# Optimization experiments

Hardware: AMD Instinct MI355X
Metric: run time of the kernel (lower is better)

Reference implementation:

```python
import jax, jax.numpy as jnp
import numpy as np

KH, KW = 3, 3
STRIDE = (1, 1)
PAD = ((1, 1), (1, 1))
WEIGHT_BIT = 8


def asym_quant_params(num_bits, smin, smax):
    # ZeroQ asymmetric_linear_quantization_params (signed, integral zero point)
    n = 2.0 ** num_bits - 1.0
    scale = n / jnp.maximum(smax - smin, 1e-8)
    zero_point = jnp.round(scale * smin) + 2.0 ** (num_bits - 1)
    return scale, zero_point


def setup_inputs() -> dict:
    key = jax.random.key(0)
    k1, k2, k3 = jax.random.split(key, 3)
    x = jax.random.normal(k1, (16, 128, 56, 56), dtype=jnp.float32)
    weight = jax.random.normal(k2, (128, 128, 3, 3), dtype=jnp.float32) * 0.05
    bias = jax.random.normal(k3, (128,), dtype=jnp.float32) * 0.1
    return {"x": x, "weight": weight, "bias": bias, "activation_bit": 8}


def reference(x, weight, bias, activation_bit):
    B, C, H, W = x.shape
    Cout = weight.shape[0]

    # nn.functional.unfold(x, 3, stride=1, padding=1).transpose(1, 2)
    # conv_general_dilated_patches emits feature dim ordered (c, kh, kw),
    # matching torch unfold's channel-major layout.
    patches = jax.lax.conv_general_dilated_patches(
        x, filter_shape=(KH, KW), window_strides=STRIDE, padding=PAD)
    _, F, OH, OW = patches.shape          # F = C*KH*KW
    L = OH * OW
    calc_x = patches.reshape(B, F, L).transpose(0, 2, 1)  # [B, L, F]

    # ----- weight quantization: per-output-channel asymmetric int8 -----
    w2 = weight.reshape(Cout, -1)                          # [Cout, F]
    w_min = w2.min(axis=1)
    w_max = w2.max(axis=1)
    scale_w, zp_w = asym_quant_params(WEIGHT_BIT, w_min, w_max)  # [Cout]
    nw = 2.0 ** (WEIGHT_BIT - 1)
    qw = jnp.clip(jnp.round(scale_w[:, None] * w2 - zp_w[:, None]), -nw, nw - 1)

    # ----- activation quantization: per-tensor asymmetric -----
    x_min = calc_x.min()
    x_max = calc_x.max()
    scale_x, zp_x = asym_quant_params(activation_bit, x_min, x_max)
    nx = 2.0 ** (activation_bit - 1)
    qx = jnp.clip(jnp.round(scale_x * calc_x - zp_x), -nx, nx - 1)  # [B, L, F]

    # bias: linear_quantize(bias, scale_w*scale_x, 0)
    qb = jnp.round(scale_w * scale_x * bias)                # [Cout]

    # integer matmul + asymmetric zero-point correction
    # real value r ~= (q + zp) / scale, so
    # x.w*sx*sw = qx.qw + zp_w*sum(qx) + zp_x*sum(qw) + K*zp_w*zp_x
    mult_res = jnp.einsum('blf,of->blo', qx, qw)            # [B, L, Cout]
    K = w2.shape[1]
    res = (mult_res
           + zp_w * qx.sum(-1, keepdims=True)               # [B, L, 1]*[Cout]
           + zp_x * qw.sum(axis=1)                          # [Cout]
           + K * zp_w * zp_x
           + qb)                                            # [B, L, Cout]

    # requantize accumulator to activation_bit bits, then dequantize
    r_min, r_max = res.min(), res.max()
    scale_r, zp_r = asym_quant_params(activation_bit, r_min, r_max)
    nr = 2.0 ** (activation_bit - 1)
    qr = jnp.clip(jnp.round(scale_r * res - zp_r), -nr, nr - 1)
    out = (qr + zp_r) / scale_r / (scale_w * scale_x)       # [B, L, Cout]

    return out.transpose(0, 2, 1)                           # [B, Cout, L]
```

## Files before the change

kernel.cpp:

```cpp
#include <hip/hip_runtime.h>
#include <stdint.h>

#pragma clang fp contract(off)

typedef __attribute__((ext_vector_type(4))) int i32x4;
typedef __attribute__((ext_vector_type(16))) int i32x16;

#define B_    16
#define C_    128
#define HW_   56
#define L_    3136
#define CO_   128
#define F_    1152
#define M_    50176
#define NT_   784

#define OFF_PBMIN 0
#define OFF_PBMAX 3136
#define OFF_PRMIN 6272
#define OFF_PRMAX 9408
#define OFF_SW    12544
#define OFF_ZPW   13056
#define OFF_CNT   14080
#define OFF_QS    15616
#define OFF_QW    16384
#define OFF_QX    163840
#define OFF_S     6586368
#define OFF_RES   6787072

__device__ __forceinline__ int read_abit(const int* p) {
    int i = *p;
    if (i > 0 && i < 32) return i;
    float f = __int_as_float(i);
    int fi = (int)f;
    return (fi > 0 && fi < 32) ? fi : 8;
}

__device__ __forceinline__ int swz_tile(int blk) {
    return (blk & 7) * 98 + (blk >> 3);
}

__device__ __forceinline__ void gsync(char* ws, int sp) {
    unsigned* base = (unsigned*)(ws + OFF_CNT) + sp * 128;
    __syncthreads();
    if (threadIdx.x == 0) {
        __threadfence();
        atomicAdd(&base[(blockIdx.x & 7) * 16], 1u);
    }
    if (threadIdx.x < 8) {
        while (__hip_atomic_load(&base[threadIdx.x * 16],
                                 __ATOMIC_RELAXED, __HIP_MEMORY_SCOPE_AGENT) < 98u)
            __builtin_amdgcn_s_sleep(2);
    }
    __threadfence();
    __syncthreads();
}

__device__ __forceinline__ void block_fminmax(float& mn, float& mx, float* sred) {
    for (int m = 32; m; m >>= 1) {
        mn = fminf(mn, __shfl_xor(mn, m));
        mx = fmaxf(mx, __shfl_xor(mx, m));
    }
    int w = threadIdx.x >> 6;
    if ((threadIdx.x & 63) == 0) { sred[w] = mn; sred[4 + w] = mx; }
    __syncthreads();
    mn = fminf(fminf(sred[0], sred[1]), fminf(sred[2], sred[3]));
    mx = fmaxf(fmaxf(sred[4], sred[5]), fmaxf(sred[6], sred[7]));
    __syncthreads();
}
__device__ __forceinline__ void block_iminmax(int& mn, int& mx, int* ired) {
    for (int m = 32; m; m >>= 1) {
        mn = min(mn, __shfl_xor(mn, m));
        mx = max(mx, __shfl_xor(mx, m));
    }
    int w = threadIdx.x >> 6;
    if ((threadIdx.x & 63) == 0) { ired[w] = mn; ired[4 + w] = mx; }
    __syncthreads();
    mn = min(min(ired[0], ired[1]), min(ired[2], ired[3]));
    mx = max(max(ired[4], ired[5]), max(ired[6], ired[7]));
    __syncthreads();
}
__device__ __forceinline__ int block_isum(int v, int* ired) {
    for (int m = 32; m; m >>= 1) v += __shfl_xor(v, m);
    int w = threadIdx.x >> 6;
    if ((threadIdx.x & 63) == 0) ired[w] = v;
    __syncthreads();
    v = ired[0] + ired[1] + ired[2] + ired[3];
    __syncthreads();
    return v;
}

__device__ __forceinline__ void dev_p1(const float4* __restrict__ x4, int n4,
                                       char* ws, float* sred) {
    float mn = 0.0f, mx = 0.0f;
    int stride = gridDim.x * blockDim.x;
    for (int i = blockIdx.x * blockDim.x + threadIdx.x; i < n4; i += stride) {
        float4 v = x4[i];
        mn = fminf(mn, fminf(fminf(v.x, v.y), fminf(v.z, v.w)));
        mx = fmaxf(mx, fmaxf(fmaxf(v.x, v.y), fmaxf(v.z, v.w)));
    }
    block_fminmax(mn, mx, sred);
    if (threadIdx.x == 0) {
        ((float*)(ws + OFF_PBMIN))[blockIdx.x] = mn;
        ((float*)(ws + OFF_PBMAX))[blockIdx.x] = mx;
    }
}

__device__ __forceinline__ void dev_p1w(const float* __restrict__ wgt,
                                        char* ws, float* sred, int* ired) {
    int o = blockIdx.x;
    const float* wr = wgt + o * F_;
    float mn = 3.4e38f, mx = -3.4e38f;
    for (int f = threadIdx.x; f < F_; f += 256) {
        float v = wr[f];
        mn = fminf(mn, v); mx = fmaxf(mx, v);
    }
    block_fminmax(mn, mx, sred);
    float sw = 255.0f / fmaxf(mx - mn, 1e-8f);
    float zw = rintf(sw * mn) + 128.0f;
    signed char* qw = (signed char*)(ws + OFF_QW);
    int qsum = 0;
    for (int f = threadIdx.x; f < F_; f += 256) {
        float q = fminf(fmaxf(rintf(sw * wr[f] - zw), -128.0f), 127.0f);
        int qi = (int)q;
        qsum += qi;
        int c = f / 9, j = f - c * 9;
        qw[j * 16384 + (c >> 4) * 2048 + (o << 4) + (c & 15)] = (signed char)qi;
    }
    qsum = block_isum(qsum, ired);
    if (threadIdx.x == 0) {
        ((int*)(ws + OFF_QS))[o]  = qsum;
        ((int*)(ws + OFF_ZPW))[o] = (int)zw;
        ((float*)(ws + OFF_SW))[o] = sw;
    }
}

__device__ __forceinline__ void dev_reduce_pb(const char* ws, float* sred,
                                              float& xmin, float& xmax) {
    const float* pbmin = (const float*)(ws + OFF_PBMIN);
    const float* pbmax = (const float*)(ws + OFF_PBMAX);
    float mn = 0.0f, mx = 0.0f;
    for (int i = threadIdx.x; i < NT_; i += 256) {
        mn = fminf(mn, pbmin[i]);
        mx = fmaxf(mx, pbmax[i]);
    }
    block_fminmax(mn, mx, sred);
    xmin = mn; xmax = mx;
}

__device__ __forceinline__ void dev_reduce_pr(const char* ws, int* ired,
                                              int& rmin, int& rmax) {
    const int* prmin = (const int*)(ws + OFF_PRMIN);
    const int* prmax = (const int*)(ws + OFF_PRMAX);
    int mn = INT32_MAX, mx = INT32_MIN;
    for (int i = threadIdx.x; i < NT_; i += 256) {
        mn = min(mn, prmin[i]);
        mx = max(mx, prmax[i]);
    }
    block_iminmax(mn, mx, ired);
    rmin = mn; rmax = mx;
}

__device__ __forceinline__ void dev_p2x(const float* __restrict__ x, char* ws, char* pool,
                                        float sx, float zx, int nx) {
    int (*ssum)[64] = (int(*)[64])pool;
    float lo = -(float)nx, hif = (float)(nx - 1);
    signed char* qxt = (signed char*)(ws + OFF_QX);
    int gid = swz_tile(blockIdx.x);
    int b = gid / 49, lcq = gid - b * 49;
    int l0 = lcq * 64;
    int t = threadIdx.x, lane = t & 63, cgp = t >> 6;
    int l = l0 + lane;
    const float* xb = x + ((size_t)b * C_) * L_ + l;
    int4* dst = (int4*)(qxt + ((size_t)(b * L_ + l)) * 128);
    int psum = 0;
    #pragma unroll
    for (int ii = 0; ii < 2; ++ii) {
        int c16 = (cgp + 4 * ii) * 16;
        int wds[4];
        #pragma unroll
        for (int k = 0; k < 4; ++k) {
            int wv = 0;
            #pragma unroll
            for (int e = 0; e < 4; ++e) {
                int c = c16 + 4 * k + e;
                float v = xb[(size_t)c * L_];
                int qi = (int)fminf(fmaxf(rintf(sx * v - zx), lo), hif);
                psum += qi;
                wv |= (qi & 255) << (8 * e);
            }
            wds[k] = wv;
        }
        int4 vv; vv.x = wds[0]; vv.y = wds[1]; vv.z = wds[2]; vv.w = wds[3];
        dst[c16 >> 4] = vv;
    }
    ssum[cgp][lane] = psum;
    __syncthreads();
    if (cgp == 0) {
        int* S = (int*)(ws + OFF_S);
        S[b * L_ + l] = ssum[0][lane] + ssum[1][lane] + ssum[2][lane] + ssum[3][lane];
    }
    __syncthreads();
}

template <bool WRITE_RES>
__device__ __forceinline__ void dev_p3(char* __restrict__ ws, char* pool, int* ired,
                                       const float* __restrict__ bias,
                                       int abit, float sx, float zx,
                                       i32x16& acc0, i32x16& acc1) {
    signed char* As = (signed char*)pool;
    signed char* Bs = (signed char*)(pool + 8192);
    int* S_s = (int*)(pool + 24576);
    int* sq  = (int*)(pool + 25504);
    const signed char* qxt = (const signed char*)(ws + OFF_QX);
    const signed char* qw  = (const signed char*)(ws + OFF_QW);
    const int* Sg  = (const int*)(ws + OFF_S);
    const int* zpw = (const int*)(ws + OFF_ZPW);

    int t = threadIdx.x;
    int mg = swz_tile(blockIdx.x) * 64;
    int b = mg / L_, l0 = mg - b * L_;
    int prow0 = l0 / HW_;
    int nx = 1 << (abit - 1);
    int q0 = min(max(-(int)zx, -nx), nx - 1);
    int pw = (q0 & 255) * 0x01010101;
    int4 pad4; pad4.x = pw; pad4.y = pw; pad4.z = pw; pad4.w = pw;
    int padS = C_ * q0;
    const signed char* qxtb = qxt + (size_t)b * L_ * 128;
    const int* Sb = Sg + b * L_;

    int chA = t & 7, rowA0 = t >> 3, rowA1 = rowA0 + 32;
    int li0 = l0 + rowA0, li1 = l0 + rowA1;
    int oh0 = li0 / HW_, ow0 = li0 - oh0 * HW_;
    int oh1 = li1 / HW_, ow1 = li1 - oh1 * HW_;

    int4 a0, a1, br0, br1, br2, br3;
    #define P3_LOAD_A(J) do {                                                          \
        int kh = (J) / 3 - 1, kw = (J) % 3 - 1;                                        \
        int ih = oh0 + kh, iw = ow0 + kw;                                              \
        a0 = ((unsigned)ih < HW_ && (unsigned)iw < HW_)                                \
             ? *(const int4*)(qxtb + ((ih * HW_ + iw) << 7) + (chA << 4)) : pad4;      \
        ih = oh1 + kh; iw = ow1 + kw;                                                  \
        a1 = ((unsigned)ih < HW_ && (unsigned)iw < HW_)                                \
             ? *(const int4*)(qxtb + ((ih * HW_ + iw) << 7) + (chA << 4)) : pad4;      \
    } while (0)
    #define P3_LOAD_B(J) do {                                                          \
        const int4* src = (const int4*)(qw + (J) * 16384);                             \
        br0 = src[t]; br1 = src[256 + t]; br2 = src[512 + t]; br3 = src[768 + t];      \
    } while (0)

    P3_LOAD_A(0); P3_LOAD_B(0);
    if (t < 232) {
        int ri = t / 58, c1 = t - ri * 58;
        int ih = prow0 - 1 + ri, iw = c1 - 1;
        S_s[t] = ((unsigned)ih < HW_ && (unsigned)iw < HW_) ? Sb[ih * HW_ + iw] : padS;
    }
    __syncthreads();
    if (t < 64) {
        int l = l0 + t;
        int oh = l / HW_, ow = l - oh * HW_;
        int ri = oh - prow0 + 1, ci = ow + 1;
        int s = 0;
        #pragma unroll
        for (int dr = -1; dr <= 1; ++dr)
            #pragma unroll
            for (int dc = -1; dc <= 1; ++dc)
                s += S_s[(ri + dr) * 58 + ci + dc];
        sq[t] = s;
    }

    int lane = t & 63, w = t >> 6;
    int wm = (w >> 1) << 5, wn = (w & 1) << 6;
    int r = lane & 31, hi = lane >> 5;
    #pragma unroll
    for (int i = 0; i < 16; ++i) { acc0[i] = 0; acc1[i] = 0; }

    #pragma unroll
    for (int j = 0; j < 9; ++j) {
        if (j > 0) __syncthreads();
        *(int4*)&As[(rowA0 << 7) + ((chA ^ (rowA0 & 7)) << 4)] = a0;
        *(int4*)&As[(rowA1 << 7) + ((chA ^ (rowA1 & 7)) << 4)] = a1;
        {
            int4* d = (int4*)Bs;
            d[t] = br0; d[256 + t] = br1; d[512 + t] = br2; d[768 + t] = br3;
        }
        if (j < 8) { P3_LOAD_A(j + 1); P3_LOAD_B(j + 1); }
        __syncthreads();
        i32x4 af[4], bf0[4], bf1[4];
        #pragma unroll
        for (int kk = 0; kk < 4; ++kk) {
            int ch2 = kk * 2 + hi, row = wm + r;
            af[kk]  = *(const i32x4*)&As[(row << 7) + ((ch2 ^ (row & 7)) << 4)];
            bf0[kk] = *(const i32x4*)&Bs[ch2 * 2048 + ((wn + r) << 4)];
            bf1[kk] = *(const i32x4*)&Bs[ch2 * 2048 + ((wn + 32 + r) << 4)];
        }
        #pragma unroll
        for (int kk = 0; kk < 4; ++kk) {
            acc0 = __builtin_amdgcn_mfma_i32_32x32x32_i8(af[kk], bf0[kk], acc0, 0, 0, 0);
            acc1 = __builtin_amdgcn_mfma_i32_32x32x32_i8(af[kk], bf1[kk], acc1, 0, 0, 0);
        }
    }
    #undef P3_LOAD_A
    #undef P3_LOAD_B

    int o0 = wn + r, o1 = wn + 32 + r;
    const int* qs = (const int*)(ws + OFF_QS);
    const float* swp = (const float*)(ws + OFF_SW);
    int zxi = (int)zx;
    int zw0 = zpw[o0], zw1 = zpw[o1];
    int c0 = zxi * qs[o0] + F_ * zw0 * zxi + (int)rintf(swp[o0] * sx * bias[o0]);
    int c1 = zxi * qs[o1] + F_ * zw1 * zxi + (int)rintf(swp[o1] * sx * bias[o1]);
    int lmin = INT32_MAX, lmax = INT32_MIN;
    int* resp = (int*)(ws + OFF_RES);
    #pragma unroll
    for (int g = 0; g < 16; ++g) {
        int row = wm + (g & 3) + ((g >> 2) << 3) + (hi << 2);
        int s = sq[row];
        int v0 = acc0[g] + zw0 * s + c0;
        int v1 = acc1[g] + zw1 * s + c1;
        acc0[g] = v0; acc1[g] = v1;
        lmin = min(lmin, min(v0, v1));
        lmax = max(lmax, max(v0, v1));
        if (WRITE_RES) {
            int m = mg + row;
            resp[m * CO_ + o0] = v0;
            resp[m * CO_ + o1] = v1;
        }
    }
    block_iminmax(lmin, lmax, ired);
    if (t == 0) {
        ((int*)(ws + OFF_PRMIN))[blockIdx.x] = lmin;
        ((int*)(ws + OFF_PRMAX))[blockIdx.x] = lmax;
    }
    __syncthreads();
}

__device__ __forceinline__ void dev_p4(const char* ws, char* pool, float* __restrict__ out,
                                       int abit, float sx, int rmin, int rmax,
                                       const i32x16& acc0, const i32x16& acc1) {
    const float* scale_w = (const float*)(ws + OFF_SW);
    float* tile = (float*)pool;
    int t = threadIdx.x;
    int mg = swz_tile(blockIdx.x) * 64;
    int b = mg / L_, l0 = mg - b * L_;
    int lane = t & 63, w = t >> 6;
    int wm = (w >> 1) << 5, wn = (w & 1) << 6;
    int r = lane & 31, hi = lane >> 5;
    int o0 = wn + r, o1 = wn + 32 + r;
    int nx = 1 << (abit - 1);
    float nlev = (float)((1 << abit) - 1);
    float rminf = (float)rmin, rmaxf = (float)rmax;
    float sr = nlev / fmaxf(rmaxf - rminf, 1e-8f);
    float zr = rintf(sr * rminf) + (float)nx;
    float lo = -(float)nx, hiq = (float)(nx - 1);
    float swsx0 = scale_w[o0] * sx, swsx1 = scale_w[o1] * sx;
    #pragma unroll
    for (int g = 0; g < 16; ++g) {
        int row = wm + (g & 3) + ((g >> 2) << 3) + (hi << 2);
        float qa = fminf(fmaxf(rintf(sr * (float)acc0[g] - zr), lo), hiq);
        float qb = fminf(fmaxf(rintf(sr * (float)acc1[g] - zr), lo), hiq);
        tile[row * 129 + o0] = ((qa + zr) / sr) / swsx0;
        tile[row * 129 + o1] = ((qb + zr) / sr) / swsx1;
    }
    __syncthreads();
    #pragma unroll
    for (int i = 0; i < 8; ++i) {
        int o = (t >> 4) + i * 16;
        int l4 = (t & 15) * 4;
        float4 f;
        #pragma unroll
        for (int jj = 0; jj < 4; ++jj)
            ((float*)&f)[jj] = tile[(l4 + jj) * 129 + o];
        *(float4*)(out + ((size_t)(b * CO_ + o)) * L_ + l0 + l4) = f;
    }
}

__global__ __launch_bounds__(256, 4) void k_fused(const float* __restrict__ x,
                                                  const float* __restrict__ wgt,
                                                  const float* __restrict__ bias,
                                                  const int* __restrict__ abit_p,
                                                  char* __restrict__ ws,
                                                  float* __restrict__ out) {
    __shared__ __align__(16) char pool[33280];
    __shared__ float sred[8];
    __shared__ int ired[8];

    int n4 = (B_ * C_ * L_) / 4;
    dev_p1((const float4*)x, n4, ws, sred);
    if (blockIdx.x < CO_) dev_p1w(wgt, ws, sred, ired);
    gsync(ws, 0);

    float xmin, xmax;
    dev_reduce_pb(ws, sred, xmin, xmax);
    int abit = read_abit(abit_p);
    float nlv = (float)((1 << abit) - 1);
    float sx = nlv / fmaxf(xmax - xmin, 1e-8f);
    float zx = rintf(sx * xmin) + (float)(1 << (abit - 1));
    int nx = 1 << (abit - 1);
    dev_p2x(x, ws, pool, sx, zx, nx);
    gsync(ws, 1);

    i32x16 acc0, acc1;
    dev_p3<false>(ws, pool, ired, bias, abit, sx, zx, acc0, acc1);
    gsync(ws, 2);

    int rmin, rmax;
    dev_reduce_pr(ws, ired, rmin, rmax);
    dev_p4(ws, pool, out, abit, sx, rmin, rmax, acc0, acc1);
}

__global__ __launch_bounds__(256) void fb_p1(const float4* __restrict__ x4, int n4,
                                             const float* __restrict__ wgt,
                                             char* __restrict__ ws) {
    __shared__ float sred[8];
    __shared__ int ired[8];
    dev_p1(x4, n4, ws, sred);
    if (blockIdx.x < CO_) dev_p1w(wgt, ws, sred, ired);
}

__global__ __launch_bounds__(256) void fb_p2(const float* __restrict__ x,
                                             const int* __restrict__ abit_p,
                                             char* __restrict__ ws) {
    __shared__ __align__(16) char pool[1024];
    __shared__ float sred[8];
    float xmin, xmax;
    dev_reduce_pb(ws, sred, xmin, xmax);
    int abit = read_abit(abit_p);
    float nlv = (float)((1 << abit) - 1);
    float sx = nlv / fmaxf(xmax - xmin, 1e-8f);
    float zx = rintf(sx * xmin) + (float)(1 << (abit - 1));
    int nx = 1 << (abit - 1);
    dev_p2x(x, ws, pool, sx, zx, nx);
}

__global__ __launch_bounds__(256, 4) void fb_p3(const float* __restrict__ bias,
                                                const int* __restrict__ abit_p,
                                                char* __restrict__ ws) {
    __shared__ __align__(16) char pool[25760];
    __shared__ float sred[8];
    __shared__ int ired[8];
    float xmin, xmax;
    dev_reduce_pb(ws, sred, xmin, xmax);
    int abit = read_abit(abit_p);
    float nlv = (float)((1 << abit) - 1);
    float sx = nlv / fmaxf(xmax - xmin, 1e-8f);
    float zx = rintf(sx * xmin) + (float)(1 << (abit - 1));
    i32x16 acc0, acc1;
    dev_p3<true>(ws, pool, ired, bias, abit, sx, zx, acc0, acc1);
}

__global__ __launch_bounds__(256) void fb_p4(const int* __restrict__ abit_p,
                                             char* __restrict__ ws,
                                             float* __restrict__ out) {
    __shared__ int tile[64 * 65];
    __shared__ float sred[8];
    __shared__ int ired[8];
    float xmin, xmax;
    dev_reduce_pb(ws, sred, xmin, xmax);
    int abit = read_abit(abit_p);
    float nlv = (float)((1 << abit) - 1);
    float sxv = nlv / fmaxf(xmax - xmin, 1e-8f);
    int rmin, rmax;
    dev_reduce_pr(ws, ired, rmin, rmax);

    const int* res = (const int*)(ws + OFF_RES);
    const float* scale_w = (const float*)(ws + OFF_SW);
    int t = threadIdx.x;
    int bid = blockIdx.x;
    int lcq = bid % 49; int tmp2 = bid / 49; int ocq = tmp2 & 1; int b = tmp2 >> 1;
    int l0 = lcq * 64, o0 = ocq * 64;

    const int* resb = res + ((size_t)(b * L_ + l0)) * CO_ + o0;
    #pragma unroll
    for (int i = 0; i < 4; ++i) {
        int lr = (t >> 4) + i * 16;
        int oc4 = (t & 15) * 4;
        int4 v = *(const int4*)(resb + lr * CO_ + oc4);
        int* d = &tile[lr * 65 + oc4];
        d[0] = v.x; d[1] = v.y; d[2] = v.z; d[3] = v.w;
    }
    int nxq = 1 << (abit - 1);
    float rminf = (float)rmin, rmaxf = (float)rmax;
    float sr = nlv / fmaxf(rmaxf - rminf, 1e-8f);
    float zr = rintf(sr * rminf) + (float)nxq;
    float lo = -(float)nxq, hiq = (float)(nxq - 1);
    __syncthreads();
    #pragma unroll
    for (int i = 0; i < 4; ++i) {
        int o = (t >> 4) + i * 16;
        int l4 = (t & 15) * 4;
        float swsx = scale_w[o0 + o] * sxv;
        float4 f;
        #pragma unroll
        for (int jj = 0; jj < 4; ++jj) {
            int rv = tile[(l4 + jj) * 65 + o];
            float q = fminf(fmaxf(rintf(sr * (float)rv - zr), lo), hiq);
            ((float*)&f)[jj] = ((q + zr) / sr) / swsx;
        }
        *(float4*)(out + ((size_t)(b * CO_ + o0 + o)) * L_ + l0 + l4) = f;
    }
}


extern "C" void kernel_launch(void* const* d_in, const int* in_sizes, int n_in,
                              void* d_out, int out_size, void* d_ws, size_t ws_size,
                              hipStream_t stream) {
    const float* x      = (const float*)d_in[0];
    const float* weight = (const float*)d_in[1];
    const float* bias   = (const float*)d_in[2];
    const int*   abit   = (const int*)d_in[3];
    float* out = (float*)d_out;
    char* ws = (char*)d_ws;

    int dev = 0;
    hipGetDevice(&dev);
    int ncu = 0;
    hipDeviceGetAttribute(&ncu, hipDeviceAttributeMultiprocessorCount, dev);
    int nb = 0;
    hipOccupancyMaxActiveBlocksPerMultiprocessor(&nb, (const void*)k_fused, 256, 0);

    if (nb > 0 && (long)nb * (long)ncu >= NT_) {
        hipMemsetAsync(ws + OFF_CNT, 0, 1536, stream);
        void* args[] = {(void*)&x, (void*)&weight, (void*)&bias,
                        (void*)&abit, (void*)&ws, (void*)&out};
        hipLaunchCooperativeKernel((const void*)k_fused, dim3(NT_), dim3(256),
                                   args, 0, stream);
    } else {
        int n4 = (B_ * C_ * L_) / 4;
        fb_p1<<<NT_, 256, 0, stream>>>((const float4*)x, n4, weight, ws);
        fb_p2<<<NT_, 256, 0, stream>>>(x, abit, ws);
        fb_p3<<<NT_, 256, 0, stream>>>(bias, abit, ws);
        fb_p4<<<1568, 256, 0, stream>>>(abit, ws, out);
    }
}
```

Measured before the change: 58.24 us.

## Split min/max and weight-quant phases out of cooperative kernel into separate launches

The input min/max reduction and the weight quantization move out of the fused cooperative kernel into two small kernels, one of which also computes sx/zx once and stores them in the workspace. The main kernel then needs one fewer grid-wide sync and no longer has every block re-reduce the per-block partials. It is also launched with a normal launch instead of hipLaunchCooperativeKernel, leaning on the occupancy check so all blocks are resident for the spin-based gsync. This trades one grid barrier for two extra kernel launches, and the non-cooperative launch risks deadlock if residency does not hold.

```diff
diff --git a/kernel.cpp b/kernel.cpp
--- a/kernel.cpp
+++ b/kernel.cpp
@@ -21,6 +21,7 @@
 #define OFF_PRMAX 9408
 #define OFF_SW    12544
 #define OFF_ZPW   13056
+#define OFF_SXZX  13568
 #define OFF_CNT   14080
 #define OFF_QS    15616
 #define OFF_QW    16384
@@ -90,12 +91,15 @@
     return v;
 }
 
-__device__ __forceinline__ void dev_p1(const float4* __restrict__ x4, int n4,
-                                       char* ws, float* sred) {
+__global__ __launch_bounds__(256) void kA1(const float4* __restrict__ x4,
+                                           char* __restrict__ ws) {
+    __shared__ float sred[8];
     float mn = 0.0f, mx = 0.0f;
-    int stride = gridDim.x * blockDim.x;
-    for (int i = blockIdx.x * blockDim.x + threadIdx.x; i < n4; i += stride) {
-        float4 v = x4[i];
+    int base = blockIdx.x * blockDim.x + threadIdx.x;
+    int stride = NT_ * 256;
+    #pragma unroll
+    for (int k = 0; k < 8; ++k) {
+        float4 v = x4[base + k * stride];
         mn = fminf(mn, fminf(fminf(v.x, v.y), fminf(v.z, v.w)));
         mx = fmaxf(mx, fmaxf(fmaxf(v.x, v.y), fmaxf(v.z, v.w)));
     }
@@ -106,8 +110,30 @@
     }
 }
 
-__device__ __forceinline__ void dev_p1w(const float* __restrict__ wgt,
-                                        char* ws, float* sred, int* ired) {
+__global__ __launch_bounds__(256) void kA2(const float* __restrict__ wgt,
+                                           const int* __restrict__ abit_p,
+                                           char* __restrict__ ws) {
+    __shared__ float sred[8];
+    __shared__ int ired[8];
+    if (blockIdx.x == CO_) {
+        const float* pbmin = (const float*)(ws + OFF_PBMIN);
+        const float* pbmax = (const float*)(ws + OFF_PBMAX);
+        float mn = 0.0f, mx = 0.0f;
+        for (int i = threadIdx.x; i < NT_; i += 256) {
+            mn = fminf(mn, pbmin[i]);
+            mx = fmaxf(mx, pbmax[i]);
+        }
+        block_fminmax(mn, mx, sred);
+        if (threadIdx.x == 0) {
+            int abit = read_abit(abit_p);
+            float nlv = (float)((1 << abit) - 1);
+            float sx = nlv / fmaxf(mx - mn, 1e-8f);
+            float zx = rintf(sx * mn) + (float)(1 << (abit - 1));
+            ((float*)(ws + OFF_SXZX))[0] = sx;
+            ((float*)(ws + OFF_SXZX))[1] = zx;
+        }
+        return;
+    }
     int o = blockIdx.x;
     const float* wr = wgt + o * F_;
     float mn = 3.4e38f, mx = -3.4e38f;
@@ -133,32 +159,6 @@
         ((int*)(ws + OFF_ZPW))[o] = (int)zw;
         ((float*)(ws + OFF_SW))[o] = sw;
     }
-}
-
-__device__ __forceinline__ void dev_reduce_pb(const char* ws, float* sred,
-                                              float& xmin, float& xmax) {
-    const float* pbmin = (const float*)(ws + OFF_PBMIN);
-    const float* pbmax = (const float*)(ws + OFF_PBMAX);
-    float mn = 0.0f, mx = 0.0f;
-    for (int i = threadIdx.x; i < NT_; i += 256) {
-        mn = fminf(mn, pbmin[i]);
-        mx = fmaxf(mx, pbmax[i]);
-    }
-    block_fminmax(mn, mx, sred);
-    xmin = mn; xmax = mx;
-}
-
-__device__ __forceinline__ void dev_reduce_pr(const char* ws, int* ired,
-                                              int& rmin, int& rmax) {
-    const int* prmin = (const int*)(ws + OFF_PRMIN);
-    const int* prmax = (const int*)(ws + OFF_PRMAX);
-    int mn = INT32_MAX, mx = INT32_MIN;
-    for (int i = threadIdx.x; i < NT_; i += 256) {
-        mn = min(mn, prmin[i]);
-        mx = max(mx, prmax[i]);
-    }
-    block_iminmax(mn, mx, ired);
-    rmin = mn; rmax = mx;
 }
 
 __device__ __forceinline__ void dev_p2x(const float* __restrict__ x, char* ws, char* pool,
@@ -333,6 +333,19 @@
         ((int*)(ws + OFF_PRMAX))[blockIdx.x] = lmax;
     }
     __syncthreads();
+}
+
+__device__ __forceinline__ void dev_reduce_pr(const char* ws, int* ired,
+                                              int& rmin, int& rmax) {
+    const int* prmin = (const int*)(ws + OFF_PRMIN);
+    const int* prmax = (const int*)(ws + OFF_PRMAX);
+    int mn = INT32_MAX, mx = INT32_MIN;
+    for (int i = threadIdx.x; i < NT_; i += 256) {
+        mn = min(mn, prmin[i]);
+        mx = max(mx, prmax[i]);
+    }
+    block_iminmax(mn, mx, ired);
+    rmin = mn; rmax = mx;
 }
 
 __device__ __forceinline__ void dev_p4(const char* ws, char* pool, float* __restrict__ out,
@@ -375,91 +388,62 @@
     }
 }
 
-__global__ __launch_bounds__(256, 4) void k_fused(const float* __restrict__ x,
-                                                  const float* __restrict__ wgt,
-                                                  const float* __restrict__ bias,
-                                                  const int* __restrict__ abit_p,
-                                                  char* __restrict__ ws,
-                                                  float* __restrict__ out) {
+__global__ __launch_bounds__(256, 4) void kB(const float* __restrict__ x,
+                                             const float* __restrict__ bias,
+                                             const int* __restrict__ abit_p,
+                                             char* __restrict__ ws,
+                                             float* __restrict__ out) {
     __shared__ __align__(16) char pool[33280];
-    __shared__ float sred[8];
     __shared__ int ired[8];
 
-    int n4 = (B_ * C_ * L_) / 4;
-    dev_p1((const float4*)x, n4, ws, sred);
-    if (blockIdx.x < CO_) dev_p1w(wgt, ws, sred, ired);
+    float sx = ((const float*)(ws + OFF_SXZX))[0];
+    float zx = ((const float*)(ws + OFF_SXZX))[1];
+    int abit = read_abit(abit_p);
+    int nx = 1 << (abit - 1);
+
+    dev_p2x(x, ws, pool, sx, zx, nx);
     gsync(ws, 0);
-
-    float xmin, xmax;
-    dev_reduce_pb(ws, sred, xmin, xmax);
-    int abit = read_abit(abit_p);
-    float nlv = (float)((1 << abit) - 1);
-    float sx = nlv / fmaxf(xmax - xmin, 1e-8f);
-    float zx = rintf(sx * xmin) + (float)(1 << (abit - 1));
-    int nx = 1 << (abit - 1);
-    dev_p2x(x, ws, pool, sx, zx, nx);
-    gsync(ws, 1);
 
     i32x16 acc0, acc1;
     dev_p3<false>(ws, pool, ired, bias, abit, sx, zx, acc0, acc1);
-    gsync(ws, 2);
+    gsync(ws, 1);
 
     int rmin, rmax;
     dev_reduce_pr(ws, ired, rmin, rmax);
     dev_p4(ws, pool, out, abit, sx, rmin, rmax, acc0, acc1);
 }
 
-__global__ __launch_bounds__(256) void fb_p1(const float4* __restrict__ x4, int n4,
-                                             const float* __restrict__ wgt,
-                                             char* __restrict__ ws) {
-    __shared__ float sred[8];
+__global__ __launch_bounds__(256) void fbB1(const float* __restrict__ x,
+                                            const int* __restrict__ abit_p,
+                                            char* __restrict__ ws) {
+    __shared__ __align__(16) char pool[1024];
+    float sx = ((const float*)(ws + OFF_SXZX))[0];
+    float zx = ((const float*)(ws + OFF_SXZX))[1];
+    int abit = read_abit(abit_p);
+    int nx = 1 << (abit - 1);
+    dev_p2x(x, ws, pool, sx, zx, nx);
+}
+
+__global__ __launch_bounds__(256, 4) void fbB2(const float* __restrict__ bias,
+                                               const int* __restrict__ abit_p,
+                                               char* __restrict__ ws) {
+    __shared__ __align__(16) char pool[25760];
     __shared__ int ired[8];
-    dev_p1(x4, n4, ws, sred);
-    if (blockIdx.x < CO_) dev_p1w(wgt, ws, sred, ired);
-}
-
-__global__ __launch_bounds__(256) void fb_p2(const float* __restrict__ x,
-                                             const int* __restrict__ abit_p,
-                                             char* __restrict__ ws) {
-    __shared__ __align__(16) char pool[1024];
-    __shared__ float sred[8];
-    float xmin, xmax;
-    dev_reduce_pb(ws, sred, xmin, xmax);
+    float sx = ((const float*)(ws + OFF_SXZX))[0];
+    float zx = ((const float*)(ws + OFF_SXZX))[1];
+    int abit = read_abit(abit_p);
+    i32x16 acc0, acc1;
+    dev_p3<true>(ws, pool, ired, bias, abit, sx, zx, acc0, acc1);
+}
+
+__global__ __launch_bounds__(256) void fbB3(const int* __restrict__ abit_p,
+                                            char* __restrict__ ws,
+                                            float* __restrict__ out) {
+    __shared__ int tile[64 * 65];
+    __shared__ int ired[8];
+    float sxv = ((const float*)(ws + OFF_SXZX))[0];
     int abit = read_abit(abit_p);
     float nlv = (float)((1 << abit) - 1);
-    float sx = nlv / fmaxf(xmax - xmin, 1e-8f);
-    float zx = rintf(sx * xmin) + (float)(1 << (abit - 1));
-    int nx = 1 << (abit - 1);
-    dev_p2x(x, ws, pool, sx, zx, nx);
-}
-
-__global__ __launch_bounds__(256, 4) void fb_p3(const float* __restrict__ bias,
-                                                const int* __restrict__ abit_p,
-                                                char* __restrict__ ws) {
-    __shared__ __align__(16) char pool[25760];
-    __shared__ float sred[8];
-    __shared__ int ired[8];
-    float xmin, xmax;
-    dev_reduce_pb(ws, sred, xmin, xmax);
-    int abit = read_abit(abit_p);
-    float nlv = (float)((1 << abit) - 1);
-    float sx = nlv / fmaxf(xmax - xmin, 1e-8f);
-    float zx = rintf(sx * xmin) + (float)(1 << (abit - 1));
-    i32x16 acc0, acc1;
-    dev_p3<true>(ws, pool, ired, bias, abit, sx, zx, acc0, acc1);
-}
-
-__global__ __launch_bounds__(256) void fb_p4(const int* __restrict__ abit_p,
-                                             char* __restrict__ ws,
-                                             float* __restrict__ out) {
-    __shared__ int tile[64 * 65];
-    __shared__ float sred[8];
-    __shared__ int ired[8];
-    float xmin, xmax;
-    dev_reduce_pb(ws, sred, xmin, xmax);
-    int abit = read_abit(abit_p);
-    float nlv = (float)((1 << abit) - 1);
-    float sxv = nlv / fmaxf(xmax - xmin, 1e-8f);
     int rmin, rmax;
     dev_reduce_pr(ws, ired, rmin, rmax);
 
@@ -517,19 +501,17 @@
     int ncu = 0;
     hipDeviceGetAttribute(&ncu, hipDeviceAttributeMultiprocessorCount, dev);
     int nb = 0;
-    hipOccupancyMaxActiveBlocksPerMultiprocessor(&nb, (const void*)k_fused, 256, 0);
+    hipOccupancyMaxActiveBlocksPerMultiprocessor(&nb, (const void*)kB, 256, 0);
+
+    kA1<<<NT_, 256, 0, stream>>>((const float4*)x, ws);
+    kA2<<<CO_ + 1, 256, 0, stream>>>(weight, abit, ws);
 
     if (nb > 0 && (long)nb * (long)ncu >= NT_) {
-        hipMemsetAsync(ws + OFF_CNT, 0, 1536, stream);
-        void* args[] = {(void*)&x, (void*)&weight, (void*)&bias,
-                        (void*)&abit, (void*)&ws, (void*)&out};
-        hipLaunchCooperativeKernel((const void*)k_fused, dim3(NT_), dim3(256),
-                                   args, 0, stream);
+        hipMemsetAsync(ws + OFF_CNT, 0, 1024, stream);
+        kB<<<NT_, 256, 0, stream>>>(x, bias, abit, ws, out);
     } else {
-        int n4 = (B_ * C_ * L_) / 4;
-        fb_p1<<<NT_, 256, 0, stream>>>((const float4*)x, n4, weight, ws);
-        fb_p2<<<NT_, 256, 0, stream>>>(x, abit, ws);
-        fb_p3<<<NT_, 256, 0, stream>>>(bias, abit, ws);
-        fb_p4<<<1568, 256, 0, stream>>>(abit, ws, out);
-    }
-}
+        fbB1<<<NT_, 256, 0, stream>>>(x, abit, ws);
+        fbB2<<<NT_, 256, 0, stream>>>(bias, abit, ws);
+        fbB3<<<1568, 256, 0, stream>>>(abit, ws, out);
+    }
+}
```

New measurement: 54.63 us. 6.2% less time.
